# Kernel optimization log

Hardware: AMD Instinct MI355X
Metric: run time of the kernel (lower is better)

The kernel has to match this reference:

```python
import jax, jax.numpy as jnp
import numpy as np

STATE_DIM = 4
CONCEPT_DIM = 8
FLOW_DIM = 3
H1, H2 = 64, 32
FLOW_LAYERS = 10
FLOW_HID = 32
TWO_PI = 6.283185307179586


def _made_masks():
    d_in = np.arange(1, FLOW_DIM + 1)                      # input degrees [1,2,3]
    d_hid = (np.arange(FLOW_HID) % (FLOW_DIM - 1)) + 1     # hidden degrees in {1,2}
    m_h = (d_hid[None, :] >= d_in[:, None]).astype(np.float32)  # (3, 32)
    m_o = (d_in[None, :] > d_hid[:, None]).astype(np.float32)   # (32, 3)
    return jnp.asarray(m_h), jnp.asarray(m_o)


def setup_inputs() -> dict:
    key = jax.random.key(0)
    ks = jax.random.split(key, 16)
    B = 2_000_000
    s = 0.1
    inp = {
        "states": jax.random.normal(ks[0], (B, STATE_DIM), dtype=jnp.float32),
        # encoder MLP 4 -> 64 -> 32 -> 8 (ReLU)
        "enc_w1": jax.random.normal(ks[1], (STATE_DIM, H1), dtype=jnp.float32) * s,
        "enc_b1": jnp.zeros((H1,), jnp.float32),
        "enc_w2": jax.random.normal(ks[2], (H1, H2), dtype=jnp.float32) * s,
        "enc_b2": jnp.zeros((H2,), jnp.float32),
        "enc_w3": jax.random.normal(ks[3], (H2, CONCEPT_DIM), dtype=jnp.float32) * s,
        "enc_b3": jnp.zeros((CONCEPT_DIM,), jnp.float32),
        # projection 8 -> 3
        "proj_w": jax.random.normal(ks[4], (CONCEPT_DIM, FLOW_DIM), dtype=jnp.float32) * s,
        "proj_b": jnp.zeros((FLOW_DIM,), jnp.float32),
        # MAF flow: 10 layers of masked MLP 3 -> 32 -> (mu, alpha)
        "flow_wh": jax.random.normal(ks[5], (FLOW_LAYERS, FLOW_DIM, FLOW_HID), dtype=jnp.float32) * s,
        "flow_bh": jnp.zeros((FLOW_LAYERS, FLOW_HID), jnp.float32),
        "flow_wmu": jax.random.normal(ks[6], (FLOW_LAYERS, FLOW_HID, FLOW_DIM), dtype=jnp.float32) * s,
        "flow_bmu": jnp.zeros((FLOW_LAYERS, FLOW_DIM), jnp.float32),
        "flow_wa": jax.random.normal(ks[7], (FLOW_LAYERS, FLOW_HID, FLOW_DIM), dtype=jnp.float32) * s,
        "flow_ba": jnp.zeros((FLOW_LAYERS, FLOW_DIM), jnp.float32),
    }
    return inp


def reference(states, enc_w1, enc_b1, enc_w2, enc_b2, enc_w3, enc_b3,
              proj_w, proj_b, flow_wh, flow_bh, flow_wmu, flow_bmu,
              flow_wa, flow_ba):
    m_h, m_o = _made_masks()
    # ConceptEncoder: MLP with ReLU
    h = jax.nn.relu(states @ enc_w1 + enc_b1)
    h = jax.nn.relu(h @ enc_w2 + enc_b2)
    concepts = h @ enc_w3 + enc_b3                      # (B, 8)
    # projection to flow dim
    x = concepts @ proj_w + proj_b                      # (B, 3)
    for l in range(FLOW_LAYERS):
        hh = jax.nn.relu(x @ (flow_wh[l] * m_h) + flow_bh[l])        # (B, 32)
        mu = hh @ (flow_wmu[l] * m_o) + flow_bmu[l]                  # (B, 3)
        alpha = jnp.tanh(hh @ (flow_wa[l] * m_o) + flow_ba[l])       # bounded log-scale
        x = (x - mu) * jnp.exp(-alpha)
        x = jnp.flip(x, axis=-1)
    # SquashingLayer: sigmoid -> unit cube (0,1)^3
    u = jax.nn.sigmoid(x)
    # ExactDiffeomorphism (vectorized across batch): unit cube -> HSV cylinder
    hue = TWO_PI * u[:, 0]
    hsv = jnp.stack([hue, u[:, 1], u[:, 2]], axis=-1)   # (B, 3)
    return hsv
```

## Files before the change

### kernel.cpp

```cpp
#include <hip/hip_runtime.h>
#include <math.h>

#define TWO_PI_F 6.283185307179586f

typedef __fp16 half2_t __attribute__((ext_vector_type(2)));
typedef __fp16 half8_t __attribute__((ext_vector_type(8)));
typedef float  f32x4   __attribute__((ext_vector_type(4)));
typedef unsigned u32x2 __attribute__((ext_vector_type(2)));

#define OFF_A1C   0
#define OFF_A2    128
#define OFF_ATL   1152
#define OFF_ENCFB 1408
#define OFF_FL    1424

__device__ __forceinline__ unsigned pack2(float a, float b) {
    half2_t h = __builtin_amdgcn_cvt_pkrtz(a, b);
    union { half2_t h; unsigned u; } cvt;
    cvt.h = h;
    return cvt.u;
}

__global__ __launch_bounds__(256)
void gsi_setup(const float* __restrict__ ew1, const float* __restrict__ ew2,
               const float* __restrict__ ew3, const float* __restrict__ eb3,
               const float* __restrict__ pw,  const float* __restrict__ pb,
               const float* __restrict__ fwh, const float* __restrict__ fbh,
               const float* __restrict__ fwmu, const float* __restrict__ fbmu,
               const float* __restrict__ fwa, const float* __restrict__ fba,
               unsigned* __restrict__ ws)
{
    int t = threadIdx.x;

    for (int idx = t; idx < 128; idx += 256) {
        int tt = idx >> 5, rest = idx & 31, m15 = rest >> 1, h = rest & 1;
        int f = 16 * tt + m15;
        ws[OFF_A1C + idx] = pack2(ew1[(2 * h) * 64 + f], ew1[(2 * h + 1) * 64 + f]);
    }
    for (int idx = t; idx < 1024; idx += 256) {
        int r = idx & 3, l = (idx >> 2) & 63, f = idx >> 8;
        int mt = f >> 1, kt = f & 1, q = l >> 4, m = (l & 15) + 16 * mt;
        int j0 = 2 * r;
        int c0 = 32 * kt + 4 * q + (j0 & 3) + 16 * (j0 >> 2);
        ws[OFF_A2 + idx] = pack2(ew2[c0 * 32 + m], ew2[(c0 + 1) * 32 + m]);
    }
    for (int idx = t; idx < 256; idx += 256) {
        int lane = idx >> 2, r = idx & 3;
        int q = lane >> 4, m15 = lane & 15;
        unsigned v = 0;
        if (m15 < 3) {
            int j0 = 2 * r, j1 = 2 * r + 1;
            int k0 = 4 * q + (j0 & 3) + 16 * (j0 >> 2);
            int k1 = 4 * q + (j1 & 3) + 16 * (j1 >> 2);
            float w0 = 0.f, w1 = 0.f;
            for (int c = 0; c < 8; ++c) {
                w0 += ew3[k0 * 8 + c] * pw[c * 3 + m15];
                w1 += ew3[k1 * 8 + c] * pw[c * 3 + m15];
            }
            v = pack2(w0, w1);
        }
        ws[OFF_ATL + idx] = v;
    }
    if (t < 3) {
        float b = pb[t];
        for (int c = 0; c < 8; ++c) b += eb3[c] * pw[c * 3 + t];
        union { float f; unsigned u; } cvt; cvt.f = b;
        ws[OFF_ENCFB + t] = cvt.u;
    }

    for (int idx = t; idx < 160; idx += 256) {
        int l = idx >> 4, j = idx & 15;
        unsigned* L = ws + OFF_FL + l * 112;
        L[j]      = pack2(fwh[l * 96 + 0 * 32 + 2 * j], fwh[l * 96 + 0 * 32 + 2 * j + 1]);
        L[16 + j] = pack2(0.0f, fwh[l * 96 + 1 * 32 + 2 * j + 1]);
        L[32 + j] = pack2(fbh[l * 32 + 2 * j], fbh[l * 32 + 2 * j + 1]);
        L[48 + j] = pack2(fwmu[l * 96 + (2 * j) * 3 + 2], fwmu[l * 96 + (2 * j + 1) * 3 + 2]);
        L[64 + j] = pack2(fwa [l * 96 + (2 * j) * 3 + 2], fwa [l * 96 + (2 * j + 1) * 3 + 2]);
    }
    for (int idx = t; idx < 80; idx += 256) {
        int l = idx >> 3, p = idx & 7;
        unsigned* L = ws + OFF_FL + l * 112;
        L[80 + p] = pack2(fwmu[l * 96 + (4 * p) * 3 + 1], fwmu[l * 96 + (4 * p + 2) * 3 + 1]);
        L[88 + p] = pack2(fwa [l * 96 + (4 * p) * 3 + 1], fwa [l * 96 + (4 * p + 2) * 3 + 1]);
    }
    if (t < 10) {
        float* Lf = (float*)(ws + OFF_FL + t * 112 + 96);
        Lf[0] = fbmu[t * 3 + 0];
        Lf[1] = fbmu[t * 3 + 1];
        Lf[2] = fbmu[t * 3 + 2];
        Lf[3] = fba[t * 3 + 1];
        Lf[4] = fba[t * 3 + 2];
        Lf[5] = expf(-tanhf(fba[t * 3 + 0]));
    }
}

__device__ __forceinline__ float fast_rcp(float x) { return __builtin_amdgcn_rcpf(x); }

__device__ __forceinline__ float fast_tanh(float x) {
    float ax = fabsf(x);
    float t = __expf(-2.0f * ax);
    float r = (1.0f - t) * fast_rcp(1.0f + t);
    return copysignf(r, x);
}

__device__ __forceinline__ unsigned relu2u(float a, float b) {
    half2_t p = __builtin_amdgcn_cvt_pkrtz(a, b);
    half2_t z = {0, 0};
    union { half2_t h; unsigned u; } cvt;
    cvt.h = __builtin_elementwise_max(p, z);
    return cvt.u;
}

__device__ __forceinline__ half8_t mk8(unsigned a, unsigned b, unsigned c, unsigned d) {
    union { unsigned u[4]; half8_t v; } r;
    r.u[0] = a; r.u[1] = b; r.u[2] = c; r.u[3] = d;
    return r.v;
}

__device__ __forceinline__ half2_t evens(half2_t lo, half2_t hi) {
    union { half2_t h; unsigned u; } a, b, r;
    a.h = hi; b.h = lo;
    r.u = __builtin_amdgcn_perm(a.u, b.u, 0x05040100u);
    return r.h;
}

__global__ __launch_bounds__(256)
void gsi_kernel(const float* __restrict__ states,
                const float* __restrict__ eb1, const float* __restrict__ eb2,
                const unsigned* __restrict__ ws,
                float* __restrict__ out, int n)
{
    int i = blockIdx.x * blockDim.x + threadIdx.x;
    int lane = threadIdx.x & 63;
    int wid = threadIdx.x >> 6;
    int rowbase = blockIdx.x * 256 + wid * 64;
    int q = lane >> 4;
    int l15 = lane & 15;
    bool q0 = (q == 0);

    const half8_t* a2p8  = (const half8_t*)(ws + OFF_A2);
    const float*   encfb = (const float*)(ws + OFF_ENCFB);

    half8_t aF1[4];
#pragma unroll
    for (int t = 0; t < 4; ++t) {
        u32x2 c = *(const u32x2*)(ws + OFF_A1C + t * 32 + l15 * 2);
        aF1[t] = mk8(q0 ? c.x : 0u, q0 ? c.y : 0u, 0u, 0u);
    }
    half8_t aF2[4];
#pragma unroll
    for (int f = 0; f < 4; ++f) aF2[f] = a2p8[f * 64 + lane];
    half8_t aFt = a2p8[4 * 64 + lane];

    f32x4 eb1c[4];
#pragma unroll
    for (int t = 0; t < 4; ++t) eb1c[t] = *(const f32x4*)(eb1 + 16 * t + 4 * q);
    f32x4 eb2c[2];
#pragma unroll
    for (int mt = 0; mt < 2; ++mt) eb2c[mt] = *(const f32x4*)(eb2 + 16 * mt + 4 * q);
    f32x4 tbias;
    {
        float e0 = encfb[0], e1 = encfb[1], e2 = encfb[2];
        tbias[0] = q0 ? e0 : 0.f;
        tbias[1] = q0 ? e1 : 0.f;
        tbias[2] = q0 ? e2 : 0.f;
        tbias[3] = 0.f;
    }

    f32x4 acct[4];
#pragma unroll
    for (int nt = 0; nt < 4; ++nt) {
        int row = rowbase + 16 * nt + l15;
        row = row < n ? row : (n - 1);
        const float4 s = reinterpret_cast<const float4*>(states)[row];
        unsigned p01 = pack2(s.x, s.y);
        unsigned p23 = pack2(s.z, s.w);
        half8_t b1 = mk8(q0 ? p01 : 0u, q0 ? p23 : 0u, 0u, 0u);

        f32x4 acc1[4];
#pragma unroll
        for (int t = 0; t < 4; ++t)
            acc1[t] = __builtin_amdgcn_mfma_f32_16x16x32_f16(aF1[t], b1, eb1c[t], 0, 0, 0);

        half8_t b2f0 = mk8(relu2u(acc1[0][0], acc1[0][1]), relu2u(acc1[0][2], acc1[0][3]),
                           relu2u(acc1[1][0], acc1[1][1]), relu2u(acc1[1][2], acc1[1][3]));
        half8_t b2f1 = mk8(relu2u(acc1[2][0], acc1[2][1]), relu2u(acc1[2][2], acc1[2][3]),
                           relu2u(acc1[3][0], acc1[3][1]), relu2u(acc1[3][2], acc1[3][3]));

        f32x4 acc2[2];
#pragma unroll
        for (int mt = 0; mt < 2; ++mt) {
            f32x4 a = __builtin_amdgcn_mfma_f32_16x16x32_f16(aF2[mt * 2 + 0], b2f0, eb2c[mt], 0, 0, 0);
            acc2[mt] = __builtin_amdgcn_mfma_f32_16x16x32_f16(aF2[mt * 2 + 1], b2f1, a, 0, 0, 0);
        }

        half8_t btl = mk8(relu2u(acc2[0][0], acc2[0][1]), relu2u(acc2[0][2], acc2[0][3]),
                          relu2u(acc2[1][0], acc2[1][1]), relu2u(acc2[1][2], acc2[1][3]));

        acct[nt] = __builtin_amdgcn_mfma_f32_16x16x32_f16(aFt, btl, tbias, 0, 0, 0);
    }

    float x0, x1, x2;
    {
        int paddr = l15 * 4;
        float xr[3];
#pragma unroll
        for (int m = 0; m < 3; ++m) {
            float p0 = __int_as_float(__builtin_amdgcn_ds_bpermute(paddr, __float_as_int(acct[0][m])));
            float p1 = __int_as_float(__builtin_amdgcn_ds_bpermute(paddr, __float_as_int(acct[1][m])));
            float p2 = __int_as_float(__builtin_amdgcn_ds_bpermute(paddr, __float_as_int(acct[2][m])));
            float p3 = __int_as_float(__builtin_amdgcn_ds_bpermute(paddr, __float_as_int(acct[3][m])));
            float lo = (lane & 32) ? p2 : p0;
            float hi = (lane & 32) ? p3 : p1;
            xr[m] = (lane & 16) ? hi : lo;
        }
        x0 = xr[0]; x1 = xr[1]; x2 = xr[2];
    }

#pragma unroll
    for (int l = 0; l < 10; ++l) {
        const unsigned* L = ws + OFF_FL + l * 112;
        const half2_t* w0p = (const half2_t*)(L);
        const half2_t* w1p = (const half2_t*)(L + 16);
        const half2_t* bhp = (const half2_t*)(L + 32);
        const half2_t* m2w = (const half2_t*)(L + 48);
        const half2_t* a2w = (const half2_t*)(L + 64);
        const half2_t* m1w = (const half2_t*)(L + 80);
        const half2_t* a1w = (const half2_t*)(L + 88);
        const float*   sc  = (const float*)(L + 96);

        half2_t x0d = __builtin_amdgcn_cvt_pkrtz(x0, x0);
        half2_t x1d = __builtin_amdgcn_cvt_pkrtz(x1, x1);
        half2_t z = {0, 0};
        half2_t hp[16];
#pragma unroll
        for (int j = 0; j < 16; ++j) {
            half2_t h = __builtin_elementwise_fma(x1d, w1p[j], bhp[j]);
            h = __builtin_elementwise_fma(x0d, w0p[j], h);
            hp[j] = __builtin_elementwise_max(h, z);
        }

        float mu1 = sc[1], mu2 = sc[2], aa1 = sc[3], aa2 = sc[4];
#pragma unroll
        for (int kk = 0; kk < 16; ++kk) {
            mu2 = __builtin_amdgcn_fdot2(hp[kk], m2w[kk], mu2, false);
            aa2 = __builtin_amdgcn_fdot2(hp[kk], a2w[kk], aa2, false);
        }
#pragma unroll
        for (int p = 0; p < 8; ++p) {
            half2_t e = evens(hp[2 * p], hp[2 * p + 1]);
            mu1 = __builtin_amdgcn_fdot2(e, m1w[p], mu1, false);
            aa1 = __builtin_amdgcn_fdot2(e, a1w[p], aa1, false);
        }

        float t1 = fast_tanh(aa1);
        float t2 = fast_tanh(aa2);
        float y0 = (x0 - sc[0]) * sc[5];
        float y1 = (x1 - mu1) * __expf(-t1);
        float y2 = (x2 - mu2) * __expf(-t2);
        x0 = y2; x1 = y1; x2 = y0;
    }

    float u0 = fast_rcp(1.0f + __expf(-x0));
    float u1 = fast_rcp(1.0f + __expf(-x1));
    float u2 = fast_rcp(1.0f + __expf(-x2));

    if (i < n) {
        out[3 * i + 0] = TWO_PI_F * u0;
        out[3 * i + 1] = u1;
        out[3 * i + 2] = u2;
    }
}

extern "C" void kernel_launch(void* const* d_in, const int* in_sizes, int n_in,
                              void* d_out, int out_size, void* d_ws, size_t ws_size,
                              hipStream_t stream) {
    const float* states = (const float*)d_in[0];
    const float* ew1  = (const float*)d_in[1];
    const float* eb1  = (const float*)d_in[2];
    const float* ew2  = (const float*)d_in[3];
    const float* eb2  = (const float*)d_in[4];
    const float* ew3  = (const float*)d_in[5];
    const float* eb3  = (const float*)d_in[6];
    const float* pw   = (const float*)d_in[7];
    const float* pb   = (const float*)d_in[8];
    const float* fwh  = (const float*)d_in[9];
    const float* fbh  = (const float*)d_in[10];
    const float* fwmu = (const float*)d_in[11];
    const float* fbmu = (const float*)d_in[12];
    const float* fwa  = (const float*)d_in[13];
    const float* fba  = (const float*)d_in[14];
    float* out = (float*)d_out;
    unsigned* ws = (unsigned*)d_ws;

    gsi_setup<<<1, 256, 0, stream>>>(ew1, ew2, ew3, eb3, pw, pb,
                                     fwh, fbh, fwmu, fbmu, fwa, fba, ws);

    int n = in_sizes[0] / 4;
    int grid = (n + 255) / 256;
    gsi_kernel<<<grid, 256, 0, stream>>>(states, eb1, eb2, ws, out, n);
}
```

Baseline: 110.7 us.

## Defer constant x0 affine step across flow layers and split hidden units even/odd

Folds the per-layer constant affine update of the first flow coordinate into the next layer's mu/alpha parameters (scaled weights, combined bias, exponent offset), leaving only one final affine after the loop. Reorganizes the hidden layer into even/odd halves so the masked zero-weight FMA for odd-degree units and the perm-based gather of even units are removed. Flow biases are staged in LDS per block, which adds a barrier and shared memory use. Relies on exact algebraic refactoring of the constant transform, with slight fp16 rounding differences from the pre-scaled weights.

```diff
diff --git a/kernel.cpp b/kernel.cpp
--- a/kernel.cpp
+++ b/kernel.cpp
@@ -13,6 +13,8 @@
 #define OFF_ATL   1152
 #define OFF_ENCFB 1408
 #define OFF_FL    1424
+#define OFF_FB    2224
+#define OFF_FIN   2464
 
 __device__ __forceinline__ unsigned pack2(float a, float b) {
     half2_t h = __builtin_amdgcn_cvt_pkrtz(a, b);
@@ -68,29 +70,43 @@
         ws[OFF_ENCFB + t] = cvt.u;
     }
 
-    for (int idx = t; idx < 160; idx += 256) {
-        int l = idx >> 4, j = idx & 15;
-        unsigned* L = ws + OFF_FL + l * 112;
-        L[j]      = pack2(fwh[l * 96 + 0 * 32 + 2 * j], fwh[l * 96 + 0 * 32 + 2 * j + 1]);
-        L[16 + j] = pack2(0.0f, fwh[l * 96 + 1 * 32 + 2 * j + 1]);
-        L[32 + j] = pack2(fbh[l * 32 + 2 * j], fbh[l * 32 + 2 * j + 1]);
-        L[48 + j] = pack2(fwmu[l * 96 + (2 * j) * 3 + 2], fwmu[l * 96 + (2 * j + 1) * 3 + 2]);
-        L[64 + j] = pack2(fwa [l * 96 + (2 * j) * 3 + 2], fwa [l * 96 + (2 * j + 1) * 3 + 2]);
-    }
     for (int idx = t; idx < 80; idx += 256) {
         int l = idx >> 3, p = idx & 7;
-        unsigned* L = ws + OFF_FL + l * 112;
-        L[80 + p] = pack2(fwmu[l * 96 + (4 * p) * 3 + 1], fwmu[l * 96 + (4 * p + 2) * 3 + 1]);
-        L[88 + p] = pack2(fwa [l * 96 + (4 * p) * 3 + 1], fwa [l * 96 + (4 * p + 2) * 3 + 1]);
+        unsigned* L = ws + OFF_FL + l * 80;
+        float invc = (l == 0) ? 1.0f : expf(tanhf(fba[(l - 1) * 3 + 0]));
+        L[p]      = pack2(fwh[l * 96 + 4 * p],          fwh[l * 96 + 4 * p + 2]);
+        L[8 + p]  = pack2(fwh[l * 96 + 4 * p + 1],      fwh[l * 96 + 4 * p + 3]);
+        L[16 + p] = pack2(fwh[l * 96 + 32 + 4 * p + 1], fwh[l * 96 + 32 + 4 * p + 3]);
+        L[24 + p] = pack2(fwmu[l * 96 + (4 * p) * 3 + 2] * invc,
+                          fwmu[l * 96 + (4 * p + 2) * 3 + 2] * invc);
+        L[32 + p] = pack2(fwmu[l * 96 + (4 * p + 1) * 3 + 2] * invc,
+                          fwmu[l * 96 + (4 * p + 3) * 3 + 2] * invc);
+        L[40 + p] = pack2(fwa[l * 96 + (4 * p) * 3 + 2],     fwa[l * 96 + (4 * p + 2) * 3 + 2]);
+        L[48 + p] = pack2(fwa[l * 96 + (4 * p + 1) * 3 + 2], fwa[l * 96 + (4 * p + 3) * 3 + 2]);
+        L[56 + p] = pack2(fwmu[l * 96 + (4 * p) * 3 + 1],    fwmu[l * 96 + (4 * p + 2) * 3 + 1]);
+        L[64 + p] = pack2(fwa[l * 96 + (4 * p) * 3 + 1],     fwa[l * 96 + (4 * p + 2) * 3 + 1]);
+    }
+    for (int idx = t; idx < 160; idx += 256) {
+        int l = idx >> 4, j = idx & 15, p = j & 7;
+        unsigned v = (j < 8) ? pack2(fbh[l * 32 + 4 * p],     fbh[l * 32 + 4 * p + 2])
+                             : pack2(fbh[l * 32 + 4 * p + 1], fbh[l * 32 + 4 * p + 3]);
+        ws[OFF_FB + l * 24 + j] = v;
     }
     if (t < 10) {
-        float* Lf = (float*)(ws + OFF_FL + t * 112 + 96);
-        Lf[0] = fbmu[t * 3 + 0];
-        Lf[1] = fbmu[t * 3 + 1];
-        Lf[2] = fbmu[t * 3 + 2];
-        Lf[3] = fba[t * 3 + 1];
-        Lf[4] = fba[t * 3 + 2];
-        Lf[5] = expf(-tanhf(fba[t * 3 + 0]));
+        int l = t;
+        float c_prev  = (l == 0) ? 1.0f : expf(-tanhf(fba[(l - 1) * 3 + 0]));
+        float bm0_prev = (l == 0) ? 0.0f : fbmu[(l - 1) * 3 + 0];
+        float* F = (float*)(ws + OFF_FB + l * 24 + 16);
+        F[0] = bm0_prev + fbmu[l * 3 + 2] / c_prev;
+        F[1] = fbmu[l * 3 + 1];
+        F[2] = fba[l * 3 + 2];
+        F[3] = fba[l * 3 + 1];
+        F[4] = (l == 0) ? 0.0f : -tanhf(fba[(l - 1) * 3 + 0]);
+    }
+    if (t == 0) {
+        float* F = (float*)(ws + OFF_FIN);
+        F[0] = fbmu[9 * 3 + 0];
+        F[1] = expf(-tanhf(fba[9 * 3 + 0]));
     }
 }
 
@@ -117,19 +133,16 @@
     return r.v;
 }
 
-__device__ __forceinline__ half2_t evens(half2_t lo, half2_t hi) {
-    union { half2_t h; unsigned u; } a, b, r;
-    a.h = hi; b.h = lo;
-    r.u = __builtin_amdgcn_perm(a.u, b.u, 0x05040100u);
-    return r.h;
-}
-
 __global__ __launch_bounds__(256)
 void gsi_kernel(const float* __restrict__ states,
                 const float* __restrict__ eb1, const float* __restrict__ eb2,
                 const unsigned* __restrict__ ws,
                 float* __restrict__ out, int n)
 {
+    __shared__ unsigned flds[240];
+    if (threadIdx.x < 240) flds[threadIdx.x] = ws[OFF_FB + threadIdx.x];
+    __syncthreads();
+
     int i = blockIdx.x * blockDim.x + threadIdx.x;
     int lane = threadIdx.x & 63;
     int wid = threadIdx.x >> 6;
@@ -219,46 +232,58 @@
 
 #pragma unroll
     for (int l = 0; l < 10; ++l) {
-        const unsigned* L = ws + OFF_FL + l * 112;
-        const half2_t* w0p = (const half2_t*)(L);
-        const half2_t* w1p = (const half2_t*)(L + 16);
-        const half2_t* bhp = (const half2_t*)(L + 32);
-        const half2_t* m2w = (const half2_t*)(L + 48);
-        const half2_t* a2w = (const half2_t*)(L + 64);
-        const half2_t* m1w = (const half2_t*)(L + 80);
-        const half2_t* a1w = (const half2_t*)(L + 88);
-        const float*   sc  = (const float*)(L + 96);
+        const half2_t* w0e = (const half2_t*)(ws + OFF_FL + l * 80);
+        const half2_t* w0o = (const half2_t*)(ws + OFF_FL + l * 80 + 8);
+        const half2_t* w1o = (const half2_t*)(ws + OFF_FL + l * 80 + 16);
+        const half2_t* m2e = (const half2_t*)(ws + OFF_FL + l * 80 + 24);
+        const half2_t* m2o = (const half2_t*)(ws + OFF_FL + l * 80 + 32);
+        const half2_t* a2e = (const half2_t*)(ws + OFF_FL + l * 80 + 40);
+        const half2_t* a2o = (const half2_t*)(ws + OFF_FL + l * 80 + 48);
+        const half2_t* m1w = (const half2_t*)(ws + OFF_FL + l * 80 + 56);
+        const half2_t* a1w = (const half2_t*)(ws + OFF_FL + l * 80 + 64);
+
+        const half2_t* bhe = (const half2_t*)(flds + l * 24);
+        const half2_t* bho = (const half2_t*)(flds + l * 24 + 8);
+        const float*   ini = (const float*)(flds + l * 24 + 16);
 
         half2_t x0d = __builtin_amdgcn_cvt_pkrtz(x0, x0);
         half2_t x1d = __builtin_amdgcn_cvt_pkrtz(x1, x1);
         half2_t z = {0, 0};
-        half2_t hp[16];
-#pragma unroll
-        for (int j = 0; j < 16; ++j) {
-            half2_t h = __builtin_elementwise_fma(x1d, w1p[j], bhp[j]);
-            h = __builtin_elementwise_fma(x0d, w0p[j], h);
-            hp[j] = __builtin_elementwise_max(h, z);
-        }
-
-        float mu1 = sc[1], mu2 = sc[2], aa1 = sc[3], aa2 = sc[4];
-#pragma unroll
-        for (int kk = 0; kk < 16; ++kk) {
-            mu2 = __builtin_amdgcn_fdot2(hp[kk], m2w[kk], mu2, false);
-            aa2 = __builtin_amdgcn_fdot2(hp[kk], a2w[kk], aa2, false);
-        }
+
+        half2_t he[8], ho[8];
 #pragma unroll
         for (int p = 0; p < 8; ++p) {
-            half2_t e = evens(hp[2 * p], hp[2 * p + 1]);
-            mu1 = __builtin_amdgcn_fdot2(e, m1w[p], mu1, false);
-            aa1 = __builtin_amdgcn_fdot2(e, a1w[p], aa1, false);
+            he[p] = __builtin_elementwise_max(
+                        __builtin_elementwise_fma(x0d, w0e[p], bhe[p]), z);
+            ho[p] = __builtin_elementwise_max(
+                        __builtin_elementwise_fma(x0d, w0o[p],
+                            __builtin_elementwise_fma(x1d, w1o[p], bho[p])), z);
+        }
+
+        float mu2 = ini[0], mu1 = ini[1], aa2 = ini[2], aa1 = ini[3];
+#pragma unroll
+        for (int p = 0; p < 8; ++p) {
+            mu2 = __builtin_amdgcn_fdot2(he[p], m2e[p], mu2, false);
+            mu2 = __builtin_amdgcn_fdot2(ho[p], m2o[p], mu2, false);
+            aa2 = __builtin_amdgcn_fdot2(he[p], a2e[p], aa2, false);
+            aa2 = __builtin_amdgcn_fdot2(ho[p], a2o[p], aa2, false);
+            mu1 = __builtin_amdgcn_fdot2(he[p], m1w[p], mu1, false);
+            aa1 = __builtin_amdgcn_fdot2(he[p], a1w[p], aa1, false);
         }
 
         float t1 = fast_tanh(aa1);
         float t2 = fast_tanh(aa2);
-        float y0 = (x0 - sc[0]) * sc[5];
-        float y1 = (x1 - mu1) * __expf(-t1);
-        float y2 = (x2 - mu2) * __expf(-t2);
-        x0 = y2; x1 = y1; x2 = y0;
+        float s2 = __expf(ini[4] - t2);
+        float s1 = __expf(-t1);
+        float y2 = (x2 - mu2) * s2;
+        float y1 = (x1 - mu1) * s1;
+        float nx2 = x0;
+        x0 = y2; x1 = y1; x2 = nx2;
+    }
+
+    {
+        const float* fin = (const float*)(ws + OFF_FIN);
+        x2 = (x2 - fin[0]) * fin[1];
     }
 
     float u0 = fast_rcp(1.0f + __expf(-x0));
```

New measurement: 98.22 us, median of 2. 11.3% less time.
